# Performance work log

Hardware: AMD Instinct MI355X
Metric: run time of the kernel (lower is better)

## Reference

```python
import jax, jax.numpy as jnp
import numpy as np
from jax import lax

VOCAB, NUM_CLASSES = 21128, 53
EMB, FILT, K = 128, 128, 3
B, L = 512, 512


def setup_inputs() -> dict:
    key = jax.random.key(0)
    ks = jax.random.split(key, 8)
    char_ids = jax.random.randint(ks[0], (B, L), 0, VOCAB, dtype=jnp.int64 if jax.config.jax_enable_x64 else jnp.int32)
    pos_e1 = jax.random.randint(ks[1], (B,), 0, L - 1, dtype=jnp.int32)
    pos_e2 = jax.random.randint(ks[2], (B,), 0, L - 1, dtype=jnp.int32)
    emb_table = jax.random.normal(ks[3], (VOCAB, EMB), dtype=jnp.float32) * 0.02
    emb_table = emb_table.at[0].set(0.0)  # padding_idx=0
    conv_w = jax.random.normal(ks[4], (FILT, EMB, K), dtype=jnp.float32) * (1.0 / np.sqrt(EMB * K))
    conv_b = jax.random.normal(ks[5], (FILT,), dtype=jnp.float32) * 0.01
    fc_w = jax.random.normal(ks[6], (NUM_CLASSES, FILT * 3), dtype=jnp.float32) * (1.0 / np.sqrt(FILT * 3))
    fc_b = jax.random.normal(ks[7], (NUM_CLASSES,), dtype=jnp.float32) * 0.01
    return {"char_ids": char_ids, "pos_e1": pos_e1, "pos_e2": pos_e2,
            "emb_table": emb_table, "conv_w": conv_w, "conv_b": conv_b,
            "fc_w": fc_w, "fc_b": fc_b}


def reference(char_ids, pos_e1, pos_e2, emb_table, conv_w, conv_b, fc_w, fc_b):
    b, seq = char_ids.shape
    x = emb_table[char_ids]                      # (b, L, E)
    x = jnp.transpose(x, (0, 2, 1))              # (b, E, L)
    conv_out = lax.conv_general_dilated(
        x, conv_w, window_strides=(1,), padding=[(K // 2, K // 2)],
        dimension_numbers=("NCH", "OIH", "NCH"))
    conv_out = jax.nn.relu(conv_out + conv_b[None, :, None])  # (b, F, L)

    # sort + clip entity boundaries, replicate e1==e2 -> e2=e1+1 adjustment
    e1 = jnp.clip(jnp.minimum(pos_e1, pos_e2), 0, seq)
    e2 = jnp.clip(jnp.maximum(pos_e1, pos_e2), 0, seq)
    e2 = jnp.where(e1 == e2, jnp.minimum(e1 + 1, seq), e2)

    idx = jnp.arange(seq)[None, :]               # (1, L)
    m1 = idx < jnp.maximum(e1, 1)[:, None]       # [:e1] or [:1] if e1==0
    m2 = (idx >= e1[:, None]) & (idx < e2[:, None])
    m3 = idx >= jnp.minimum(e2, seq - 1)[:, None]  # [e2:] or last col if e2==L

    neg = jnp.float32(-jnp.inf)
    def seg_max(mask):
        return jnp.max(jnp.where(mask[:, None, :], conv_out, neg), axis=-1)  # (b, F)

    pooled = jnp.concatenate([seg_max(m1), seg_max(m2), seg_max(m3)], axis=-1)  # (b, 3F)
    return pooled @ fc_w.T + fc_b
```

## Files before the change

kernel.cpp:

```cpp
#include <hip/hip_runtime.h>
#include <stdint.h>

#define VOCAB 21128
#define NUMC  53
#define EMB   128
#define SEQ   512
#define BATCH 512

typedef __bf16 bf16x8 __attribute__((ext_vector_type(8)));
typedef float f32x4 __attribute__((ext_vector_type(4)));

__device__ __forceinline__ unsigned short f2bf(float f) {
    union { float f; unsigned int u; } v; v.f = f;
    unsigned int r = (v.u + 0x7FFFu + ((v.u >> 16) & 1u)) >> 16;
    return (unsigned short)r;
}

__global__ void prep_kernel(const float* __restrict__ emb, const float* __restrict__ cw,
                            unsigned short* __restrict__ Tb, unsigned short* __restrict__ Wp) {
    int idx = blockIdx.x * blockDim.x + threadIdx.x;
    if (idx < VOCAB * EMB) Tb[idx] = f2bf(emb[idx]);
    if (idx < 12 * 8 * 64 * 8) {
        int j = idx & 7, l = (idx >> 3) & 63, g = (idx >> 9) & 7, s = idx >> 12;
        int kk = s * 32 + (l >> 4) * 8 + j;
        int f = g * 16 + (l & 15);
        int tap = kk >> 7, e = kk & 127;
        Wp[idx] = f2bf(cw[(f * EMB + e) * 3 + tap]);
    }
}

__launch_bounds__(512, 2)
__global__ void pcnn_main(const int* __restrict__ cid, const int* __restrict__ p1,
                          const int* __restrict__ p2,
                          const unsigned short* __restrict__ Tb,
                          const unsigned short* __restrict__ Wp,
                          const float* __restrict__ cb, const float* __restrict__ fcw,
                          const float* __restrict__ fcb, float* __restrict__ out) {
    __shared__ __align__(16) unsigned short xs[130 * 136];
    __shared__ float pstage[8][3][128];
    __shared__ float pooled[384];
    __shared__ float fcred[53][4];

    const int b    = blockIdx.x;
    const int tid  = threadIdx.x;
    const int lane = tid & 63;
    const int w    = tid >> 6;
    const int wm   = w & 1;
    const int wn   = w >> 1;
    const int quad = lane >> 4;
    const int lc   = lane & 15;

    bf16x8 bfr[12][2];
#pragma unroll
    for (int s = 0; s < 12; ++s)
#pragma unroll
        for (int nt = 0; nt < 2; ++nt) {
            int g = wn * 2 + nt;
            bfr[s][nt] = *(const bf16x8*)(Wp + (size_t)((s * 8 + g) * 64 + lane) * 8);
        }

    int e1 = min(p1[b], p2[b]);
    int e2 = max(p1[b], p2[b]);
    if (e1 == e2) e2 = min(e1 + 1, SEQ);
    const int e1m = max(e1, 1);

    float smax[3][2];
#pragma unroll
    for (int s3 = 0; s3 < 3; ++s3) { smax[s3][0] = -1e30f; smax[s3][1] = -1e30f; }

    const int* crow = cid + (size_t)b * SEQ;

    for (int t = 0; t < 4; ++t) {
        __syncthreads();
        {
            const int c = tid & 15;
            for (int r = tid >> 4; r < 130; r += 32) {
                int gp = t * 128 + r - 1;
                uint4 val = make_uint4(0u, 0u, 0u, 0u);
                if (gp >= 0 && gp < SEQ) {
                    int id = crow[gp];
                    val = *(const uint4*)(Tb + (size_t)id * EMB + c * 8);
                }
                *(uint4*)(xs + r * 136 + c * 8) = val;
            }
        }
        __syncthreads();

        f32x4 acc[4][2];
#pragma unroll
        for (int mt = 0; mt < 4; ++mt)
#pragma unroll
            for (int nt = 0; nt < 2; ++nt)
                acc[mt][nt] = (f32x4){0.f, 0.f, 0.f, 0.f};

#pragma unroll
        for (int s = 0; s < 12; ++s) {
            const int tap = s >> 2;
            const int eb  = (s & 3) * 32;
            bf16x8 af[4];
#pragma unroll
            for (int mt = 0; mt < 4; ++mt) {
                int r = wm * 64 + mt * 16 + lc + tap;
                af[mt] = *(const bf16x8*)(xs + r * 136 + eb + quad * 8);
            }
#pragma unroll
            for (int mt = 0; mt < 4; ++mt)
#pragma unroll
                for (int nt = 0; nt < 2; ++nt)
                    acc[mt][nt] = __builtin_amdgcn_mfma_f32_16x16x32_bf16(
                        af[mt], bfr[s][nt], acc[mt][nt], 0, 0, 0);
        }

#pragma unroll
        for (int mt = 0; mt < 4; ++mt)
#pragma unroll
            for (int reg = 0; reg < 4; ++reg) {
                int p = t * 128 + wm * 64 + mt * 16 + quad * 4 + reg;
                float a0 = (p < e1m) ? 0.f : -2e30f;
                float a1 = (p >= e1 && p < e2) ? 0.f : -2e30f;
                float a2 = (p >= e2) ? 0.f : -2e30f;
#pragma unroll
                for (int nt = 0; nt < 2; ++nt) {
                    float v = acc[mt][nt][reg];
                    smax[0][nt] = fmaxf(smax[0][nt], v + a0);
                    smax[1][nt] = fmaxf(smax[1][nt], v + a1);
                    smax[2][nt] = fmaxf(smax[2][nt], v + a2);
                }
            }
    }

    {
        int slot = wm * 4 + quad;
#pragma unroll
        for (int s3 = 0; s3 < 3; ++s3)
#pragma unroll
            for (int nt = 0; nt < 2; ++nt)
                pstage[slot][s3][(wn * 2 + nt) * 16 + lc] = smax[s3][nt];
    }
    __syncthreads();
    for (int j = tid; j < 384; j += 512) {
        int s3 = j >> 7, f = j & 127;
        float m = pstage[0][s3][f];
#pragma unroll
        for (int sl = 1; sl < 8; ++sl) m = fmaxf(m, pstage[sl][s3][f]);
        pooled[j] = fmaxf(m + cb[f], 0.f);
    }
    __syncthreads();

    if (tid < 212) {
        int c = tid >> 2, q = tid & 3;
        const float* wrow = fcw + (size_t)c * 384 + q * 96;
        const float* pp   = pooled + q * 96;
        float sum = 0.f;
#pragma unroll 8
        for (int i = 0; i < 96; ++i) sum += wrow[i] * pp[i];
        fcred[c][q] = sum;
    }
    __syncthreads();
    if (tid < NUMC)
        out[(size_t)b * NUMC + tid] =
            fcred[tid][0] + fcred[tid][1] + fcred[tid][2] + fcred[tid][3] + fcb[tid];
}

extern "C" void kernel_launch(void* const* d_in, const int* in_sizes, int n_in,
                              void* d_out, int out_size, void* d_ws, size_t ws_size,
                              hipStream_t stream) {
    const int*   cid = (const int*)d_in[0];
    const int*   p1  = (const int*)d_in[1];
    const int*   p2  = (const int*)d_in[2];
    const float* emb = (const float*)d_in[3];
    const float* cw  = (const float*)d_in[4];
    const float* cb  = (const float*)d_in[5];
    const float* fcw = (const float*)d_in[6];
    const float* fcb = (const float*)d_in[7];
    float* out = (float*)d_out;

    unsigned short* Tb = (unsigned short*)d_ws;
    unsigned short* Wp = (unsigned short*)((char*)d_ws + (size_t)VOCAB * EMB * 2);

    const int prep_threads = 256;
    const int prep_blocks  = (VOCAB * EMB + prep_threads - 1) / prep_threads;
    prep_kernel<<<prep_blocks, prep_threads, 0, stream>>>(emb, cw, Tb, Wp);
    pcnn_main<<<BATCH, 512, 0, stream>>>(cid, p1, p2, Tb, Wp, cb, fcw, fcb, out);
}
```

Measured before the change: 130.6 us.

## Double-buffer embedding gather, stage token ids in LDS, vectorize bf16 prep

The embedding conversion kernel now converts eight floats per thread with vector loads and stores instead of one element per thread. The main kernel stages pre-scaled token ids in shared memory and double-buffers the embedding tile. The next tile is gathered into registers while the MFMA convolution runs on the current one, which removes the per-tile barrier pair and the dependent id loads. The final pooling reduction now uses wave shuffles before the cross-wave LDS step. Launch bounds are raised to 4 blocks per CU, which tightens the register budget while the preloaded weight fragments and prefetch registers add pressure, so spills are a risk; the larger LDS footprint caps residency anyway.

```diff
diff --git a/kernel.cpp b/kernel.cpp
--- a/kernel.cpp
+++ b/kernel.cpp
@@ -10,36 +10,49 @@
 typedef __bf16 bf16x8 __attribute__((ext_vector_type(8)));
 typedef float f32x4 __attribute__((ext_vector_type(4)));
 
-__device__ __forceinline__ unsigned short f2bf(float f) {
+__device__ __forceinline__ unsigned int f2bf1(float f) {
     union { float f; unsigned int u; } v; v.f = f;
-    unsigned int r = (v.u + 0x7FFFu + ((v.u >> 16) & 1u)) >> 16;
-    return (unsigned short)r;
+    return (v.u + 0x7FFFu + ((v.u >> 16) & 1u)) >> 16;
+}
+__device__ __forceinline__ unsigned int pack2(float a, float b) {
+    return f2bf1(a) | (f2bf1(b) << 16);
 }
 
 __global__ void prep_kernel(const float* __restrict__ emb, const float* __restrict__ cw,
                             unsigned short* __restrict__ Tb, unsigned short* __restrict__ Wp) {
     int idx = blockIdx.x * blockDim.x + threadIdx.x;
-    if (idx < VOCAB * EMB) Tb[idx] = f2bf(emb[idx]);
+    const int n8 = VOCAB * EMB / 8;
+    if (idx < n8) {
+        const float4* src = (const float4*)emb + (size_t)idx * 2;
+        float4 a = src[0], b = src[1];
+        uint4 o;
+        o.x = pack2(a.x, a.y);
+        o.y = pack2(a.z, a.w);
+        o.z = pack2(b.x, b.y);
+        o.w = pack2(b.z, b.w);
+        *(uint4*)(Tb + (size_t)idx * 8) = o;
+    }
     if (idx < 12 * 8 * 64 * 8) {
         int j = idx & 7, l = (idx >> 3) & 63, g = (idx >> 9) & 7, s = idx >> 12;
         int kk = s * 32 + (l >> 4) * 8 + j;
         int f = g * 16 + (l & 15);
         int tap = kk >> 7, e = kk & 127;
-        Wp[idx] = f2bf(cw[(f * EMB + e) * 3 + tap]);
-    }
-}
-
-__launch_bounds__(512, 2)
+        Wp[idx] = (unsigned short)f2bf1(cw[(f * EMB + e) * 3 + tap]);
+    }
+}
+
+__launch_bounds__(512, 4)
 __global__ void pcnn_main(const int* __restrict__ cid, const int* __restrict__ p1,
                           const int* __restrict__ p2,
                           const unsigned short* __restrict__ Tb,
                           const unsigned short* __restrict__ Wp,
                           const float* __restrict__ cb, const float* __restrict__ fcw,
                           const float* __restrict__ fcb, float* __restrict__ out) {
-    __shared__ __align__(16) unsigned short xs[130 * 136];
-    __shared__ float pstage[8][3][128];
+    __shared__ __align__(16) unsigned short xs[2][130 * 136];
+    __shared__ unsigned int sid[514];
+    __shared__ float pstage[2][3][128];
     __shared__ float pooled[384];
-    __shared__ float fcred[53][4];
+    __shared__ float fcred[NUMC][4];
 
     const int b    = blockIdx.x;
     const int tid  = threadIdx.x;
@@ -50,6 +63,12 @@
     const int quad = lane >> 4;
     const int lc   = lane & 15;
 
+    for (int i = tid; i < 514; i += 512) {
+        int gp = i - 1;
+        unsigned int id = (gp >= 0 && gp < SEQ) ? (unsigned int)cid[(size_t)b * SEQ + gp] : 0u;
+        sid[i] = id * 256u;
+    }
+
     bf16x8 bfr[12][2];
 #pragma unroll
     for (int s = 0; s < 12; ++s)
@@ -68,24 +87,36 @@
 #pragma unroll
     for (int s3 = 0; s3 < 3; ++s3) { smax[s3][0] = -1e30f; smax[s3][1] = -1e30f; }
 
-    const int* crow = cid + (size_t)b * SEQ;
+    const char* TbB = (const char*)Tb;
+    const int cc = tid & 15;
+    const int r0 = tid >> 4;
+
+    __syncthreads();
+
+    uint4 g[5];
+#pragma unroll
+    for (int i = 0; i < 5; ++i) {
+        int r = r0 + 32 * i;
+        if (r < 130) g[i] = *(const uint4*)(TbB + sid[r] + cc * 16);
+    }
+#pragma unroll
+    for (int i = 0; i < 5; ++i) {
+        int r = r0 + 32 * i;
+        if (r < 130) *(uint4*)(&xs[0][r * 136 + cc * 8]) = g[i];
+    }
 
     for (int t = 0; t < 4; ++t) {
         __syncthreads();
-        {
-            const int c = tid & 15;
-            for (int r = tid >> 4; r < 130; r += 32) {
-                int gp = t * 128 + r - 1;
-                uint4 val = make_uint4(0u, 0u, 0u, 0u);
-                if (gp >= 0 && gp < SEQ) {
-                    int id = crow[gp];
-                    val = *(const uint4*)(Tb + (size_t)id * EMB + c * 8);
-                }
-                *(uint4*)(xs + r * 136 + c * 8) = val;
-            }
-        }
-        __syncthreads();
-
+
+        if (t < 3) {
+#pragma unroll
+            for (int i = 0; i < 5; ++i) {
+                int r = r0 + 32 * i;
+                if (r < 130) g[i] = *(const uint4*)(TbB + sid[(t + 1) * 128 + r] + cc * 16);
+            }
+        }
+
+        const unsigned short* xb = xs[t & 1];
         f32x4 acc[4][2];
 #pragma unroll
         for (int mt = 0; mt < 4; ++mt)
@@ -101,7 +132,7 @@
 #pragma unroll
             for (int mt = 0; mt < 4; ++mt) {
                 int r = wm * 64 + mt * 16 + lc + tap;
-                af[mt] = *(const bf16x8*)(xs + r * 136 + eb + quad * 8);
+                af[mt] = *(const bf16x8*)(xb + r * 136 + eb + quad * 8);
             }
 #pragma unroll
             for (int mt = 0; mt < 4; ++mt)
@@ -127,23 +158,38 @@
                     smax[2][nt] = fmaxf(smax[2][nt], v + a2);
                 }
             }
-    }
-
-    {
-        int slot = wm * 4 + quad;
+
+        if (t < 3) {
+#pragma unroll
+            for (int i = 0; i < 5; ++i) {
+                int r = r0 + 32 * i;
+                if (r < 130) *(uint4*)(&xs[(t + 1) & 1][r * 136 + cc * 8]) = g[i];
+            }
+        }
+    }
+
+#pragma unroll
+    for (int s3 = 0; s3 < 3; ++s3)
+#pragma unroll
+        for (int nt = 0; nt < 2; ++nt) {
+            float v = smax[s3][nt];
+            v = fmaxf(v, __shfl_xor(v, 16));
+            v = fmaxf(v, __shfl_xor(v, 32));
+            smax[s3][nt] = v;
+        }
+    if (lane < 16) {
 #pragma unroll
         for (int s3 = 0; s3 < 3; ++s3)
 #pragma unroll
             for (int nt = 0; nt < 2; ++nt)
-                pstage[slot][s3][(wn * 2 + nt) * 16 + lc] = smax[s3][nt];
-    }
-    __syncthreads();
-    for (int j = tid; j < 384; j += 512) {
-        int s3 = j >> 7, f = j & 127;
-        float m = pstage[0][s3][f];
-#pragma unroll
-        for (int sl = 1; sl < 8; ++sl) m = fmaxf(m, pstage[sl][s3][f]);
-        pooled[j] = fmaxf(m + cb[f], 0.f);
+                pstage[wm][s3][(wn * 2 + nt) * 16 + lc] = smax[s3][nt];
+    }
+    __syncthreads();
+
+    if (tid < 384) {
+        int s3 = tid >> 7, f = tid & 127;
+        float m = fmaxf(pstage[0][s3][f], pstage[1][s3][f]);
+        pooled[tid] = fmaxf(m + cb[f], 0.f);
     }
     __syncthreads();
 
@@ -178,8 +224,9 @@
     unsigned short* Tb = (unsigned short*)d_ws;
     unsigned short* Wp = (unsigned short*)((char*)d_ws + (size_t)VOCAB * EMB * 2);
 
+    const int n8 = VOCAB * EMB / 8;
     const int prep_threads = 256;
-    const int prep_blocks  = (VOCAB * EMB + prep_threads - 1) / prep_threads;
+    const int prep_blocks  = (n8 + prep_threads - 1) / prep_threads;
     prep_kernel<<<prep_blocks, prep_threads, 0, stream>>>(emb, cw, Tb, Wp);
     pcnn_main<<<BATCH, 512, 0, stream>>>(cid, p1, p2, Tb, Wp, cb, fcw, fcb, out);
 }
```

Result: slower. 157.3 us (+20.5%).
